# Optimization experiments

Measured on AMD Instinct MI355X. Metric: run time of the kernel, lower is better.

## Reference

```python
import math
import jax, jax.numpy as jnp
import numpy as np

L, B, D, Z, H, N = 2048, 8, 1024, 128, 2048, 16
MAXPOS = 2048
LAPLACE_MU, LAPLACE_SIGMA = 0.707107, 0.282095


def setup_inputs() -> dict:
    key = jax.random.key(0)
    ks = jax.random.split(key, 14)
    def rn(k, shp, s=1.0):
        return jax.random.normal(k, shp, dtype=jnp.float32) * s
    return {
        "x": rn(ks[0], (L, B, D)),
        # MultiHeadEMA params (unidirectional: kernel_dim == D)
        "delta": rn(ks[1], (D, N, 1), 0.2),
        "alpha": rn(ks[2], (D, N, 1), 0.2),
        "beta_ema": rn(ks[3], (D, N, 1), 0.02) + 1.0,
        "gamma_ema": rn(ks[4], (D, N)),
        "omega": rn(ks[5], (D,)),
        # projections
        "v_w": rn(ks[6], (D, H), 0.02), "v_b": jnp.zeros((H,), jnp.float32),
        "mx_w": rn(ks[7], (D, Z + H + 2 * D), 0.02),
        "mx_b": jnp.zeros((Z + H + 2 * D,), jnp.float32),
        "h_w": rn(ks[8], (H, D), 0.02), "h_b": jnp.zeros((D,), jnp.float32),
        # q/k affine from shared z
        "qk_gamma": rn(ks[9], (2, Z), 0.1) + 1.0,
        "qk_beta": rn(ks[10], (2, Z), 0.1),
        # simple relative positional bias
        "rel_pos": rn(ks[11], (2 * MAXPOS - 1,), 0.02),
        # prenorm layernorm
        "ln_w": jnp.ones((D,), jnp.float32),
        "ln_b": jnp.zeros((D,), jnp.float32),
    }


def _laplace(x):
    x = (x - LAPLACE_MU) / (LAPLACE_SIGMA * math.sqrt(2.0))
    return 0.5 * (1.0 + jax.lax.erf(x))


def _layer_norm(x, w, b, eps=1e-5):
    mu = jnp.mean(x, axis=-1, keepdims=True)
    var = jnp.mean(jnp.square(x - mu), axis=-1, keepdims=True)
    return (x - mu) * jax.lax.rsqrt(var + eps) * w + b


def _rel_bias(rel_pos, seq_len):
    # SimpleRelativePositionalBias: Toeplitz (L, L) matrix from a 2L-1 vector
    bvec = rel_pos[MAXPOS - seq_len:MAXPOS + seq_len - 1]  # (2L-1,)
    t = jnp.pad(bvec, (0, seq_len))                         # (3L-1,)
    t = jnp.tile(t, seq_len)[:-seq_len].reshape(seq_len, 3 * seq_len - 2)
    r = (2 * seq_len - 1) // 2
    return t[:, r:t.shape[1] - r]                           # (L, L)


def _ema_conv(xn, delta, alpha, beta_ema, gamma_ema, omega, seq_len):
    # xn: (L, B, D) -> silu(EMA(xn) + xn * omega), via FFT convolution
    scale = 1.0 / math.sqrt(N)
    p = jax.nn.sigmoid(delta)                 # (D, N, 1)
    q = 1.0 - p * jax.nn.sigmoid(alpha)       # (D, N, 1)
    vander = jnp.arange(seq_len, dtype=jnp.float32)[None, None, :] * jnp.log(q)  # (D, N, L)
    kernel = jnp.einsum('dnl,dn->dl', p * beta_ema * jnp.exp(vander), gamma_ema * scale)  # (D, L)
    residual = xn * omega                     # (L, B, D)
    xt = jnp.transpose(xn, (1, 2, 0))         # (B, D, L)
    nfft = 2 * seq_len
    kf = jnp.fft.rfft(kernel, n=nfft)         # (D, L+1) complex
    xf = jnp.fft.rfft(xt, n=nfft)             # (B, D, L+1)
    out = jnp.fft.irfft(xf * kf, n=nfft)[..., :seq_len]  # (B, D, L)
    return jax.nn.silu(jnp.transpose(out, (2, 0, 1)) + residual)  # (L, B, D)


def reference(x, delta, alpha, beta_ema, gamma_ema, omega,
              v_w, v_b, mx_w, mx_b, h_w, h_b,
              qk_gamma, qk_beta, rel_pos, ln_w, ln_b):
    seq_len = x.shape[0]
    residual = x
    xn = _layer_norm(x, ln_w, ln_b)                       # prenorm
    v = jax.nn.silu(xn @ v_w + v_b)                        # (L, B, H)
    mx = _ema_conv(xn, delta, alpha, beta_ema, gamma_ema, omega, seq_len)  # (L, B, D)
    base = mx @ mx_w + mx_b                                # (L, B, D+Z+H+D)
    u = jax.nn.sigmoid(base[..., :D])                      # update gate (L, B, D)
    zr = jax.nn.silu(base[..., D:D + Z + H])
    hx = base[..., D + Z + H:]                             # (L, B, D)
    z = zr[..., :Z]                                        # (L, B, Z)
    r = zr[..., Z:]                                        # (L, B, H)
    zqk = z[..., None, :] * qk_gamma + qk_beta             # (L, B, 2, Z)
    q = jnp.transpose(zqk[..., 0, :], (1, 0, 2))           # (B, L, Z)
    k = jnp.transpose(zqk[..., 1, :], (1, 0, 2))           # (B, L, Z)
    vb = jnp.transpose(v, (1, 0, 2))                       # (B, L, H)
    bias = _rel_bias(rel_pos, seq_len)                     # (L, L)
    qk = jnp.einsum('blz,bmz->blm', q, k) / seq_len + bias # (B, L, L)
    attn = _laplace(qk)
    h = jnp.einsum('blm,bmh->blh', attn, vb)               # (B, L, H)
    h = jnp.transpose(h, (1, 0, 2))                        # (L, B, H)
    h = jax.nn.silu(hx + (h * r) @ h_w + h_b)              # (L, B, D)
    out = residual + u * (h - residual)
    return out
```

## Files before the change

### kernel.cpp

```cpp
#include <hip/hip_runtime.h>
#include <hip/hip_bf16.h>
#include <math.h>

typedef unsigned short u16;
typedef unsigned int   u32;
typedef __bf16 bf16x8_t __attribute__((ext_vector_type(8)));
typedef float  f32x4_t  __attribute__((ext_vector_type(4)));

#define DEVI static __device__ __forceinline__

DEVI float bf2f(u16 u){ union{u32 i; float f;} v; v.i = ((u32)u)<<16; return v.f; }
DEVI u16 f2bf(float f){ union{float f; u32 i;} v; v.f = f; u32 i = v.i; i += 0x7fffu + ((i>>16)&1u); return (u16)(i>>16); }
DEVI float sigm(float x){ return 1.0f/(1.0f + __expf(-x)); }
DEVI float silu_(float x){ return x * sigm(x); }

DEVI void gload16(const u16* gsrc, u16* lds){
  __builtin_amdgcn_global_load_lds(
      (const __attribute__((address_space(1))) unsigned int*)gsrc,
      (__attribute__((address_space(3))) unsigned int*)lds, 16, 0, 0);
}

constexpr int L_=2048, B_=8, D_=1024, Z_=128, H_=2048, N_=16;
constexpr int CH_=128, NC_=16;
constexpr int MXN_=4224;

__global__ __launch_bounds__(256) void k_ln(const float* __restrict__ x,
                                            const float* __restrict__ w,
                                            const float* __restrict__ b,
                                            u16* __restrict__ xn){
  int row = blockIdx.x, t = threadIdx.x;
  int l = row >> 3, bb = row & 7;
  const float4* xr = (const float4*)(x + (size_t)row*D_);
  float4 v = xr[t];
  float s  = v.x+v.y+v.z+v.w;
  float sq = v.x*v.x+v.y*v.y+v.z*v.z+v.w*v.w;
  #pragma unroll
  for (int m=1; m<64; m<<=1){ s += __shfl_xor(s, m); sq += __shfl_xor(sq, m); }
  __shared__ float ss[4], sv[4];
  int wv = t>>6;
  if ((t&63)==0){ ss[wv]=s; sv[wv]=sq; }
  __syncthreads();
  s = ss[0]+ss[1]+ss[2]+ss[3]; sq = sv[0]+sv[1]+sv[2]+sv[3];
  float mu = s*(1.0f/D_);
  float var = sq*(1.0f/D_) - mu*mu;
  float rs = rsqrtf(var + 1e-5f);
  float4 wv4 = ((const float4*)w)[t];
  float4 bv4 = ((const float4*)b)[t];
  u16 o0 = f2bf((v.x-mu)*rs*wv4.x+bv4.x);
  u16 o1 = f2bf((v.y-mu)*rs*wv4.y+bv4.y);
  u16 o2 = f2bf((v.z-mu)*rs*wv4.z+bv4.z);
  u16 o3 = f2bf((v.w-mu)*rs*wv4.w+bv4.w);
  *(uint2*)(xn + ((size_t)bb*L_ + l)*D_ + t*4) =
      make_uint2((u32)o0 | ((u32)o1<<16), (u32)o2 | ((u32)o3<<16));
}

__global__ __launch_bounds__(256) void k_tr(const float* __restrict__ in, int R, int C,
                                            u16* __restrict__ out){
  __shared__ u16 TT[32*33];
  int c0 = blockIdx.x*32, r0 = blockIdx.y*32;
  int t = threadIdx.x;
  int lr = t>>3, lc4 = (t&7)*4;
  float4 v = *(const float4*)&in[(size_t)(r0+lr)*C + c0 + lc4];
  TT[(lc4+0)*33 + lr] = f2bf(v.x);
  TT[(lc4+1)*33 + lr] = f2bf(v.y);
  TT[(lc4+2)*33 + lr] = f2bf(v.z);
  TT[(lc4+3)*33 + lr] = f2bf(v.w);
  __syncthreads();
  int orr = t>>3, oc4 = (t&7)*4;
  u16 a0 = TT[orr*33 + oc4+0], a1 = TT[orr*33 + oc4+1];
  u16 a2 = TT[orr*33 + oc4+2], a3 = TT[orr*33 + oc4+3];
  *(uint2*)&out[(size_t)(c0+orr)*R + r0 + oc4] =
      make_uint2((u32)a0 | ((u32)a1<<16), (u32)a2 | ((u32)a3<<16));
}

__global__ void k_ema_params(const float* __restrict__ delta, const float* __restrict__ alpha,
                             const float* __restrict__ beta,  const float* __restrict__ gamma,
                             float* __restrict__ qA, float* __restrict__ wcA, float* __restrict__ qPA){
  int i = blockIdx.x*256 + threadIdx.x;
  if (i >= D_*N_) return;
  float p = 1.0f/(1.0f + expf(-delta[i]));
  float q = 1.0f - p*(1.0f/(1.0f + expf(-alpha[i])));
  qA[i]  = q;
  wcA[i] = p*beta[i]*gamma[i]*0.25f;
  qPA[i] = powf(q, (float)CH_);
}

__global__ __launch_bounds__(256) void k_ema_a(const u16* __restrict__ xn,
                                               const float* __restrict__ qA,
                                               float* __restrict__ F){
  int d = blockIdx.x*256 + threadIdx.x;
  int b = blockIdx.y, c = blockIdx.z;
  float q[N_], s[N_];
  #pragma unroll
  for (int n=0;n<N_;n++){ q[n]=qA[d*N_+n]; s[n]=0.0f; }
  for (int t=0;t<CH_;t++){
    int l = c*CH_ + t;
    float x = bf2f(xn[((size_t)b*L_ + l)*D_ + d]);
    #pragma unroll
    for (int n=0;n<N_;n++) s[n] = q[n]*s[n] + x;
  }
  float* Fo = F + (((size_t)c*B_ + b)*D_ + d)*N_;
  #pragma unroll
  for (int n=0;n<N_;n++) Fo[n] = s[n];
}

__global__ __launch_bounds__(256) void k_ema_b(float* __restrict__ F,
                                               const float* __restrict__ qPA){
  int i = blockIdx.x*256 + threadIdx.x;
  int n = i & (N_-1);
  int d = (i>>4) & (D_-1);
  int b = i >> 14;
  float qP = qPA[d*N_+n];
  float S = 0.0f;
  for (int c=0;c<NC_;c++){
    size_t idx = (((size_t)c*B_ + b)*D_ + d)*N_ + n;
    float f = F[idx];
    F[idx] = S;
    S = qP*S + f;
  }
}

__global__ __launch_bounds__(256) void k_ema_c(const u16* __restrict__ xn,
                                               const float* __restrict__ qA,
                                               const float* __restrict__ wcA,
                                               const float* __restrict__ CY,
                                               const float* __restrict__ omega,
                                               u16* __restrict__ mx){
  int d = blockIdx.x*256 + threadIdx.x;
  int b = blockIdx.y, c = blockIdx.z;
  float q[N_], wc[N_], s[N_];
  const float* cy = CY + (((size_t)c*B_ + b)*D_ + d)*N_;
  #pragma unroll
  for (int n=0;n<N_;n++){ q[n]=qA[d*N_+n]; wc[n]=wcA[d*N_+n]; s[n]=cy[n]; }
  float om = omega[d];
  for (int t=0;t<CH_;t++){
    int l = c*CH_ + t;
    float x = bf2f(xn[((size_t)b*L_ + l)*D_ + d]);
    float acc = 0.0f;
    #pragma unroll
    for (int n=0;n<N_;n++){ s[n] = q[n]*s[n] + x; acc += wc[n]*s[n]; }
    mx[((size_t)b*L_ + l)*D_ + d] = f2bf(silu_(acc + x*om));
  }
}

#define STG(BUF, K0) do {                                                         \
    int _ab = (BUF)*16384;                                                        \
    _Pragma("unroll")                                                             \
    for (int it=0; it<4; ++it){                                                   \
      int idx = it*256 + tid; int r = idx>>3, ch = idx&7;                         \
      gload16(Ab + (size_t)(rowBase + r)*lda + (K0) + ((ch ^ (r&7))*8),           \
              &LDS[_ab + idx*8]);                                                 \
    }                                                                             \
    _Pragma("unroll")                                                             \
    for (int it=0; it<4; ++it){                                                   \
      int idx = it*256 + tid; int r = idx>>3, ch = idx&7;                         \
      gload16(Bb + (size_t)(colBase + r)*ldb + (K0) + ((ch ^ (r&7))*8),           \
              &LDS[_ab + 8192 + idx*8]);                                          \
    }                                                                             \
  } while(0)

#define CMP(BUF) do {                                                             \
    int _ab = (BUF)*16384;                                                        \
    _Pragma("unroll")                                                             \
    for (int ks=0; ks<2; ++ks){                                                   \
      bf16x8_t af[4], bfr[4];                                                     \
      int kfx = (ks*32 + lane4*8) ^ ((lane15&7)<<3);                              \
      _Pragma("unroll")                                                           \
      for (int m=0;m<4;m++)                                                       \
        af[m]  = *(const bf16x8_t*)&LDS[_ab + (wm + m*16 + lane15)*64 + kfx];     \
      _Pragma("unroll")                                                           \
      for (int n=0;n<4;n++)                                                       \
        bfr[n] = *(const bf16x8_t*)&LDS[_ab + 8192 + (wn + n*16 + lane15)*64 + kfx]; \
      __builtin_amdgcn_s_setprio(1);                                              \
      _Pragma("unroll")                                                           \
      for (int m=0;m<4;m++)                                                       \
        _Pragma("unroll")                                                         \
        for (int n=0;n<4;n++)                                                     \
          acc[m][n] = __builtin_amdgcn_mfma_f32_16x16x32_bf16(af[m], bfr[n], acc[m][n], 0,0,0); \
      __builtin_amdgcn_s_setprio(0);                                              \
    }                                                                             \
  } while(0)

template<int OP>
__global__ __launch_bounds__(256) void k_gall(
    const u16* __restrict__ A, int lda, long aStr,
    const u16* __restrict__ Bm, int ldb, long bStr,
    int K,
    u16* __restrict__ C, int ldc, long cStr,
    const float* __restrict__ biasC, const float* __restrict__ biasR,
    const float* __restrict__ relpos,
    const float* __restrict__ qkg, const float* __restrict__ qkb,
    u16* __restrict__ P0, u16* __restrict__ P1,
    u16* __restrict__ P2, u16* __restrict__ P3,
    const u16* __restrict__ RP0, const u16* __restrict__ RP1,
    const float* __restrict__ xin, float* __restrict__ outf, int bb)
{
  __shared__ u16 LDS[32768];
  int zz = blockIdx.z;
  const u16* Ab = A + (size_t)zz*aStr;
  const u16* Bb = Bm + (size_t)zz*bStr;

  int gx = gridDim.x;
  int f = blockIdx.x + gx*blockIdx.y;
  int q8 = (gx*gridDim.y) >> 3;
  int wg = (f & 7)*q8 + (f >> 3);
  int rowBase = (wg / gx)*128;
  int colBase = (wg % gx)*128;

  int tid = threadIdx.x;
  int lane = tid & 63, wave = tid >> 6;
  int wm = (wave>>1)*64, wn = (wave&1)*64;
  int lane15 = lane & 15, lane4 = lane >> 4;

  f32x4_t acc[4][4];
  #pragma unroll
  for (int m=0;m<4;m++)
    #pragma unroll
    for (int n=0;n<4;n++) acc[m][n] = (f32x4_t){0.f,0.f,0.f,0.f};

  int nt = K >> 6;
  STG(0, 0);
  STG(1, 64);
  for (int t = 0; t < nt; ++t){
    if (t + 1 < nt) { asm volatile("s_waitcnt vmcnt(8)" ::: "memory"); }
    else            { asm volatile("s_waitcnt vmcnt(0)" ::: "memory"); }
    __builtin_amdgcn_s_barrier();
    __builtin_amdgcn_sched_barrier(0);
    CMP(t & 1);
    if (t + 2 < nt) {
      __builtin_amdgcn_s_barrier();
      STG(t & 1, (t+2)*64);
    }
  }

  u16* Cb  = C  ? C  + (size_t)zz*cStr : nullptr;
  u16* P0b = P0 ? P0 + (size_t)zz*((size_t)L_*D_) : nullptr;
  u16* P1b = P1 ? P1 + (size_t)zz*((size_t)L_*D_) : nullptr;
  u16* P2b = P2 ? P2 + (size_t)zz*((size_t)L_*Z_) : nullptr;
  u16* P3b = P3 ? P3 + (size_t)zz*((size_t)L_*Z_) : nullptr;
  const u16* RP0b = RP0 ? RP0 + (size_t)zz*(OP==3 ? (size_t)L_*H_ : (size_t)L_*D_) : nullptr;
  const u16* RP1b = RP1 ? RP1 + (size_t)zz*((size_t)L_*D_) : nullptr;
  int bglob = bb + zz;

  #pragma unroll
  for (int m=0;m<4;m++) {
    #pragma unroll
    for (int n=0;n<4;n++) {
      int col = colBase + wn + n*16 + lane15;
      #pragma unroll
      for (int r2=0;r2<4;r2++) {
        int row = rowBase + wm + m*16 + lane4*4 + r2;
        float v = acc[m][n][r2];
        if (OP == 0) {
          Cb[(size_t)row*ldc + col] = f2bf(silu_(v + biasR[row]));
        } else if (OP == 1) {
          v += biasC[col];
          if (col < 1024) {
            P0b[(size_t)row*1024 + col] = f2bf(sigm(v));
          } else if (col < 1152) {
            float s = silu_(v);
            int zi = col - 1024;
            P2b[(size_t)row*128 + zi] = f2bf(s*qkg[zi]     + qkb[zi]);
            P3b[(size_t)row*128 + zi] = f2bf(s*qkg[128+zi] + qkb[128+zi]);
          } else if (col < 3200) {
            Cb[(size_t)row*2048 + (col-1152)] = f2bf(silu_(v));
          } else {
            P1b[(size_t)row*1024 + (col-3200)] = f2bf(v);
          }
        } else if (OP == 2) {
          v = v*(1.0f/(float)L_) + relpos[2047 + col - row];
          v = 0.5f*(1.0f + erff((v - 0.707107f)*2.5066282746f));
          Cb[(size_t)row*ldc + col] = f2bf(v);
        } else if (OP == 3) {
          v *= bf2f(RP0b[(size_t)row*ldc + col]);
          Cb[(size_t)row*ldc + col] = f2bf(v);
        } else {
          v += biasC[col];
          float hx = bf2f(RP0b[(size_t)row*1024 + col]);
          float hval = silu_(hx + v);
          size_t gi = ((size_t)row*B_ + bglob)*D_ + col;
          float xv = xin[gi];
          float uu = bf2f(RP1b[(size_t)row*1024 + col]);
          outf[gi] = xv + uu*(hval - xv);
        }
      }
    }
  }
}

extern "C" void kernel_launch(void* const* d_in, const int* in_sizes, int n_in,
                              void* d_out, int out_size, void* d_ws, size_t ws_size,
                              hipStream_t stream) {
  const float* x      = (const float*)d_in[0];
  const float* delta  = (const float*)d_in[1];
  const float* alpha  = (const float*)d_in[2];
  const float* betaE  = (const float*)d_in[3];
  const float* gammaE = (const float*)d_in[4];
  const float* omega  = (const float*)d_in[5];
  const float* v_w    = (const float*)d_in[6];
  const float* v_b    = (const float*)d_in[7];
  const float* mx_w   = (const float*)d_in[8];
  const float* mx_b   = (const float*)d_in[9];
  const float* h_w    = (const float*)d_in[10];
  const float* h_b    = (const float*)d_in[11];
  const float* qkg    = (const float*)d_in[12];
  const float* qkb    = (const float*)d_in[13];
  const float* relpos = (const float*)d_in[14];
  const float* ln_w   = (const float*)d_in[15];
  const float* ln_b   = (const float*)d_in[16];
  float* out = (float*)d_out;

  const size_t fixedB = 92733440ull;
  const size_t perNB  = 42991616ull;
  int NB = 8;
  while (NB > 1 && fixedB + (size_t)NB*perNB > ws_size) NB >>= 1;
  int NG = B_ / NB;

  char* ws = (char*)d_ws;
  size_t o = 0;
  auto alloc = [&](size_t sz){ size_t r = o; o += sz; return r; };
  u16* XN    = (u16*)(ws + alloc(33554432));
  u16* MX    = (u16*)(ws + alloc(33554432));
  u16* VWT   = (u16*)(ws + alloc(4194304));
  u16* MXWT  = (u16*)(ws + alloc((size_t)MXN_*D_*2));
  u16* HWT   = (u16*)(ws + alloc(4194304));
  float* EQ  = (float*)(ws + alloc(65536));
  float* EW  = (float*)(ws + alloc(65536));
  float* EP  = (float*)(ws + alloc(65536));
  float* Ff  = (float*)(ws + alloc(8388608));
  u16* VT    = (u16*)(ws + alloc((size_t)NB*8388608));
  u16* ATTN  = (u16*)(ws + alloc((size_t)NB*8388608));
  u16* Rb    = (u16*)(ws + alloc((size_t)NB*8388608));
  u16* HRb   = (u16*)(ws + alloc((size_t)NB*8388608));
  u16* Ub    = (u16*)(ws + alloc((size_t)NB*4194304));
  u16* HXb   = (u16*)(ws + alloc((size_t)NB*4194304));
  u16* Qb    = (u16*)(ws + alloc((size_t)NB*524288));
  u16* Kb    = (u16*)(ws + alloc((size_t)NB*524288));

  k_ln<<<L_*B_, 256, 0, stream>>>(x, ln_w, ln_b, XN);
  k_ema_params<<<(D_*N_+255)/256, 256, 0, stream>>>(delta, alpha, betaE, gammaE, EQ, EW, EP);
  k_ema_a<<<dim3(D_/256, B_, NC_), 256, 0, stream>>>(XN, EQ, Ff);
  k_ema_b<<<(B_*D_*N_)/256, 256, 0, stream>>>(Ff, EP);
  k_ema_c<<<dim3(D_/256, B_, NC_), 256, 0, stream>>>(XN, EQ, EW, Ff, omega, MX);
  k_tr<<<dim3(H_/32, D_/32), 256, 0, stream>>>(v_w, D_, H_, VWT);
  k_tr<<<dim3(MXN_/32, D_/32), 256, 0, stream>>>(mx_w, D_, MXN_, MXWT);
  k_tr<<<dim3(D_/32, H_/32), 256, 0, stream>>>(h_w, H_, D_, HWT);

  for (int g = 0; g < NG; ++g) {
    int b0 = g*NB;
    k_gall<0><<<dim3(L_/128, H_/128, NB), 256, 0, stream>>>(
        VWT, D_, 0L, XN + (size_t)b0*L_*D_, D_, (long)L_*D_, D_,
        VT, L_, (long)H_*L_,
        nullptr, v_b, nullptr, nullptr, nullptr,
        nullptr, nullptr, nullptr, nullptr,
        nullptr, nullptr, nullptr, nullptr, 0);
    k_gall<1><<<dim3(MXN_/128, L_/128, NB), 256, 0, stream>>>(
        MX + (size_t)b0*L_*D_, D_, (long)L_*D_, MXWT, D_, 0L, D_,
        Rb, H_, (long)L_*H_,
        mx_b, nullptr, nullptr, qkg, qkb,
        Ub, HXb, Qb, Kb,
        nullptr, nullptr, nullptr, nullptr, 0);
    k_gall<2><<<dim3(L_/128, L_/128, NB), 256, 0, stream>>>(
        Qb, Z_, (long)L_*Z_, Kb, Z_, (long)L_*Z_, Z_,
        ATTN, L_, (long)L_*L_,
        nullptr, nullptr, relpos, nullptr, nullptr,
        nullptr, nullptr, nullptr, nullptr,
        nullptr, nullptr, nullptr, nullptr, 0);
    k_gall<3><<<dim3(H_/128, L_/128, NB), 256, 0, stream>>>(
        ATTN, L_, (long)L_*L_, VT, L_, (long)H_*L_, L_,
        HRb, H_, (long)L_*H_,
        nullptr, nullptr, nullptr, nullptr, nullptr,
        nullptr, nullptr, nullptr, nullptr,
        Rb, nullptr, nullptr, nullptr, 0);
    k_gall<4><<<dim3(D_/128, L_/128, NB), 256, 0, stream>>>(
        HRb, H_, (long)L_*H_, HWT, H_, 0L, H_,
        nullptr, 0, 0L,
        h_b, nullptr, nullptr, nullptr, nullptr,
        nullptr, nullptr, nullptr, nullptr,
        HXb, Ub, x, out, b0);
  }
}
```

Baseline: 741.2 us.

## Add 256x256-tile 1024-thread GEMM kernel for value, mx and attention-V GEMMs

Adds a k_g2 GEMM variant that uses 256x256 output tiles, 16 waves per block and a 128 KB double-buffered LDS staging area. It replaces the 128x128 kernel for the value projection, the mx projection and the attn@V GEMM. The goal is more operand reuse per block and less global/L2 traffic per MFMA. To make the mx GEMM tile evenly, the transposed mx weight is padded to 4352 columns. The padded columns are never written, so they hold uninitialized data, but stores for those columns are masked. The trade-off is one block per CU, fewer blocks in the grid, and more tail imbalance.

```diff
diff --git a/kernel.cpp b/kernel.cpp
--- a/kernel.cpp
+++ b/kernel.cpp
@@ -22,7 +22,7 @@
 
 constexpr int L_=2048, B_=8, D_=1024, Z_=128, H_=2048, N_=16;
 constexpr int CH_=128, NC_=16;
-constexpr int MXN_=4224;
+constexpr int MXN_=4224, MXNP_=4352;
 
 __global__ __launch_bounds__(256) void k_ln(const float* __restrict__ x,
                                             const float* __restrict__ w,
@@ -143,6 +143,137 @@
   }
 }
 
+#define STG2(BUF, K0) do {                                                        \
+    int _ab = (BUF)*32768;                                                        \
+    _Pragma("unroll")                                                             \
+    for (int it=0; it<2; ++it){                                                   \
+      int idx = it*1024 + tid; int r = idx>>3, ch = idx&7;                        \
+      gload16(Ab + (size_t)(rowBase + r)*lda + (K0) + ((ch ^ (r&7))*8),           \
+              &LDS[_ab + idx*8]);                                                 \
+    }                                                                             \
+    _Pragma("unroll")                                                             \
+    for (int it=0; it<2; ++it){                                                   \
+      int idx = it*1024 + tid; int r = idx>>3, ch = idx&7;                        \
+      gload16(Bb + (size_t)(colBase + r)*ldb + (K0) + ((ch ^ (r&7))*8),           \
+              &LDS[_ab + 16384 + idx*8]);                                         \
+    }                                                                             \
+  } while(0)
+
+#define CMP2(BUF) do {                                                            \
+    int _ab = (BUF)*32768;                                                        \
+    _Pragma("unroll")                                                             \
+    for (int ks=0; ks<2; ++ks){                                                   \
+      bf16x8_t af[4], bfr[4];                                                     \
+      int kfx = (ks*32 + lane4*8) ^ ((lane15&7)<<3);                              \
+      _Pragma("unroll")                                                           \
+      for (int m=0;m<4;m++)                                                       \
+        af[m]  = *(const bf16x8_t*)&LDS[_ab + (wr*64 + m*16 + lane15)*64 + kfx];  \
+      _Pragma("unroll")                                                           \
+      for (int n=0;n<4;n++)                                                       \
+        bfr[n] = *(const bf16x8_t*)&LDS[_ab + 16384 + (wc*64 + n*16 + lane15)*64 + kfx]; \
+      __builtin_amdgcn_s_setprio(1);                                              \
+      _Pragma("unroll")                                                           \
+      for (int m=0;m<4;m++)                                                       \
+        _Pragma("unroll")                                                         \
+        for (int n=0;n<4;n++)                                                     \
+          acc[m][n] = __builtin_amdgcn_mfma_f32_16x16x32_bf16(af[m], bfr[n], acc[m][n], 0,0,0); \
+      __builtin_amdgcn_s_setprio(0);                                              \
+    }                                                                             \
+  } while(0)
+
+template<int OP>
+__global__ __launch_bounds__(1024, 4) void k_g2(
+    const u16* __restrict__ A, int lda, long aStr,
+    const u16* __restrict__ Bm, int ldb, long bStr,
+    int K,
+    u16* __restrict__ C, int ldc, long cStr,
+    const float* __restrict__ biasC, const float* __restrict__ biasR,
+    const float* __restrict__ qkg, const float* __restrict__ qkb,
+    u16* __restrict__ P0, u16* __restrict__ P1,
+    u16* __restrict__ P2, u16* __restrict__ P3,
+    const u16* __restrict__ RP0)
+{
+  __shared__ u16 LDS[65536];
+  int zz = blockIdx.z;
+  const u16* Ab = A + (size_t)zz*aStr;
+  const u16* Bb = Bm + (size_t)zz*bStr;
+
+  int gx = gridDim.x;
+  int f = blockIdx.x + gx*blockIdx.y;
+  int q8 = (gx*gridDim.y) >> 3;
+  int wg = (f & 7)*q8 + (f >> 3);
+  int rowBase = (wg / gx)*256;
+  int colBase = (wg % gx)*256;
+
+  int tid = threadIdx.x;
+  int lane = tid & 63, wave = tid >> 6;
+  int wr = wave >> 2, wc = wave & 3;
+  int lane15 = lane & 15, lane4 = lane >> 4;
+
+  f32x4_t acc[4][4];
+  #pragma unroll
+  for (int m=0;m<4;m++)
+    #pragma unroll
+    for (int n=0;n<4;n++) acc[m][n] = (f32x4_t){0.f,0.f,0.f,0.f};
+
+  int nt = K >> 6;
+  STG2(0, 0);
+  STG2(1, 64);
+  for (int t = 0; t < nt; ++t){
+    if (t + 1 < nt) { asm volatile("s_waitcnt vmcnt(4)" ::: "memory"); }
+    else            { asm volatile("s_waitcnt vmcnt(0)" ::: "memory"); }
+    __builtin_amdgcn_s_barrier();
+    __builtin_amdgcn_sched_barrier(0);
+    CMP2(t & 1);
+    if (t + 2 < nt) {
+      __builtin_amdgcn_s_barrier();
+      STG2(t & 1, (t+2)*64);
+    }
+  }
+
+  u16* Cb  = C  ? C  + (size_t)zz*cStr : nullptr;
+  u16* P0b = P0 ? P0 + (size_t)zz*((size_t)L_*D_) : nullptr;
+  u16* P1b = P1 ? P1 + (size_t)zz*((size_t)L_*D_) : nullptr;
+  u16* P2b = P2 ? P2 + (size_t)zz*((size_t)L_*Z_) : nullptr;
+  u16* P3b = P3 ? P3 + (size_t)zz*((size_t)L_*Z_) : nullptr;
+  const u16* RP0b = RP0 ? RP0 + (size_t)zz*((size_t)L_*H_) : nullptr;
+
+  #pragma unroll
+  for (int m=0;m<4;m++) {
+    #pragma unroll
+    for (int n=0;n<4;n++) {
+      int col = colBase + wc*64 + n*16 + lane15;
+      #pragma unroll
+      for (int r2=0;r2<4;r2++) {
+        int row = rowBase + wr*64 + m*16 + lane4*4 + r2;
+        float v = acc[m][n][r2];
+        if (OP == 0) {
+          Cb[(size_t)row*ldc + col] = f2bf(silu_(v + biasR[row]));
+        } else if (OP == 1) {
+          if (col < MXN_) {
+            v += biasC[col];
+            if (col < 1024) {
+              P0b[(size_t)row*1024 + col] = f2bf(sigm(v));
+            } else if (col < 1152) {
+              float s = silu_(v);
+              int zi = col - 1024;
+              P2b[(size_t)row*128 + zi] = f2bf(s*qkg[zi]     + qkb[zi]);
+              P3b[(size_t)row*128 + zi] = f2bf(s*qkg[128+zi] + qkb[128+zi]);
+            } else if (col < 3200) {
+              Cb[(size_t)row*2048 + (col-1152)] = f2bf(silu_(v));
+            } else {
+              P1b[(size_t)row*1024 + (col-3200)] = f2bf(v);
+            }
+          }
+        } else {
+          v *= bf2f(RP0b[(size_t)row*ldc + col]);
+          Cb[(size_t)row*ldc + col] = f2bf(v);
+        }
+      }
+    }
+  }
+}
+
 #define STG(BUF, K0) do {                                                         \
     int _ab = (BUF)*16384;                                                        \
     _Pragma("unroll")                                                             \
@@ -187,11 +318,8 @@
     const u16* __restrict__ Bm, int ldb, long bStr,
     int K,
     u16* __restrict__ C, int ldc, long cStr,
-    const float* __restrict__ biasC, const float* __restrict__ biasR,
+    const float* __restrict__ biasC,
     const float* __restrict__ relpos,
-    const float* __restrict__ qkg, const float* __restrict__ qkb,
-    u16* __restrict__ P0, u16* __restrict__ P1,
-    u16* __restrict__ P2, u16* __restrict__ P3,
     const u16* __restrict__ RP0, const u16* __restrict__ RP1,
     const float* __restrict__ xin, float* __restrict__ outf, int bb)
 {
@@ -233,12 +361,8 @@
     }
   }
 
-  u16* Cb  = C  ? C  + (size_t)zz*cStr : nullptr;
-  u16* P0b = P0 ? P0 + (size_t)zz*((size_t)L_*D_) : nullptr;
-  u16* P1b = P1 ? P1 + (size_t)zz*((size_t)L_*D_) : nullptr;
-  u16* P2b = P2 ? P2 + (size_t)zz*((size_t)L_*Z_) : nullptr;
-  u16* P3b = P3 ? P3 + (size_t)zz*((size_t)L_*Z_) : nullptr;
-  const u16* RP0b = RP0 ? RP0 + (size_t)zz*(OP==3 ? (size_t)L_*H_ : (size_t)L_*D_) : nullptr;
+  u16* Cb = C ? C + (size_t)zz*cStr : nullptr;
+  const u16* RP0b = RP0 ? RP0 + (size_t)zz*((size_t)L_*D_) : nullptr;
   const u16* RP1b = RP1 ? RP1 + (size_t)zz*((size_t)L_*D_) : nullptr;
   int bglob = bb + zz;
 
@@ -251,28 +375,9 @@
       for (int r2=0;r2<4;r2++) {
         int row = rowBase + wm + m*16 + lane4*4 + r2;
         float v = acc[m][n][r2];
-        if (OP == 0) {
-          Cb[(size_t)row*ldc + col] = f2bf(silu_(v + biasR[row]));
-        } else if (OP == 1) {
-          v += biasC[col];
-          if (col < 1024) {
-            P0b[(size_t)row*1024 + col] = f2bf(sigm(v));
-          } else if (col < 1152) {
-            float s = silu_(v);
-            int zi = col - 1024;
-            P2b[(size_t)row*128 + zi] = f2bf(s*qkg[zi]     + qkb[zi]);
-            P3b[(size_t)row*128 + zi] = f2bf(s*qkg[128+zi] + qkb[128+zi]);
-          } else if (col < 3200) {
-            Cb[(size_t)row*2048 + (col-1152)] = f2bf(silu_(v));
-          } else {
-            P1b[(size_t)row*1024 + (col-3200)] = f2bf(v);
-          }
-        } else if (OP == 2) {
+        if (OP == 2) {
           v = v*(1.0f/(float)L_) + relpos[2047 + col - row];
           v = 0.5f*(1.0f + erff((v - 0.707107f)*2.5066282746f));
-          Cb[(size_t)row*ldc + col] = f2bf(v);
-        } else if (OP == 3) {
-          v *= bf2f(RP0b[(size_t)row*ldc + col]);
           Cb[(size_t)row*ldc + col] = f2bf(v);
         } else {
           v += biasC[col];
@@ -310,7 +415,7 @@
   const float* ln_b   = (const float*)d_in[16];
   float* out = (float*)d_out;
 
-  const size_t fixedB = 92733440ull;
+  const size_t fixedB = 92995584ull;
   const size_t perNB  = 42991616ull;
   int NB = 8;
   while (NB > 1 && fixedB + (size_t)NB*perNB > ws_size) NB >>= 1;
@@ -322,7 +427,7 @@
   u16* XN    = (u16*)(ws + alloc(33554432));
   u16* MX    = (u16*)(ws + alloc(33554432));
   u16* VWT   = (u16*)(ws + alloc(4194304));
-  u16* MXWT  = (u16*)(ws + alloc((size_t)MXN_*D_*2));
+  u16* MXWT  = (u16*)(ws + alloc((size_t)MXNP_*D_*2));
   u16* HWT   = (u16*)(ws + alloc(4194304));
   float* EQ  = (float*)(ws + alloc(65536));
   float* EW  = (float*)(ws + alloc(65536));
@@ -348,35 +453,28 @@
 
   for (int g = 0; g < NG; ++g) {
     int b0 = g*NB;
-    k_gall<0><<<dim3(L_/128, H_/128, NB), 256, 0, stream>>>(
+    k_g2<0><<<dim3(L_/256, H_/256, NB), 1024, 0, stream>>>(
         VWT, D_, 0L, XN + (size_t)b0*L_*D_, D_, (long)L_*D_, D_,
         VT, L_, (long)H_*L_,
-        nullptr, v_b, nullptr, nullptr, nullptr,
-        nullptr, nullptr, nullptr, nullptr,
-        nullptr, nullptr, nullptr, nullptr, 0);
-    k_gall<1><<<dim3(MXN_/128, L_/128, NB), 256, 0, stream>>>(
+        nullptr, v_b, nullptr, nullptr,
+        nullptr, nullptr, nullptr, nullptr, nullptr);
+    k_g2<1><<<dim3(MXNP_/256, L_/256, NB), 1024, 0, stream>>>(
         MX + (size_t)b0*L_*D_, D_, (long)L_*D_, MXWT, D_, 0L, D_,
         Rb, H_, (long)L_*H_,
-        mx_b, nullptr, nullptr, qkg, qkb,
-        Ub, HXb, Qb, Kb,
-        nullptr, nullptr, nullptr, nullptr, 0);
+        mx_b, nullptr, qkg, qkb,
+        Ub, HXb, Qb, Kb, nullptr);
     k_gall<2><<<dim3(L_/128, L_/128, NB), 256, 0, stream>>>(
         Qb, Z_, (long)L_*Z_, Kb, Z_, (long)L_*Z_, Z_,
         ATTN, L_, (long)L_*L_,
-        nullptr, nullptr, relpos, nullptr, nullptr,
-        nullptr, nullptr, nullptr, nullptr,
-        nullptr, nullptr, nullptr, nullptr, 0);
-    k_gall<3><<<dim3(H_/128, L_/128, NB), 256, 0, stream>>>(
+        nullptr, relpos, nullptr, nullptr, nullptr, nullptr, 0);
+    k_g2<3><<<dim3(H_/256, L_/256, NB), 1024, 0, stream>>>(
         ATTN, L_, (long)L_*L_, VT, L_, (long)H_*L_, L_,
         HRb, H_, (long)L_*H_,
-        nullptr, nullptr, nullptr, nullptr, nullptr,
         nullptr, nullptr, nullptr, nullptr,
-        Rb, nullptr, nullptr, nullptr, 0);
+        nullptr, nullptr, nullptr, nullptr, Rb);
     k_gall<4><<<dim3(D_/128, L_/128, NB), 256, 0, stream>>>(
         HRb, H_, (long)L_*H_, HWT, H_, 0L, H_,
         nullptr, 0, 0L,
-        h_b, nullptr, nullptr, nullptr, nullptr,
-        nullptr, nullptr, nullptr, nullptr,
-        HXb, Ub, x, out, b0);
-  }
-}
+        h_b, nullptr, HXb, Ub, x, out, b0);
+  }
+}
```

Result: no change. 745.5 us (+0.6%).
